# Performance work log

Hardware: AMD Instinct MI355X
Metric: run time of the kernel (lower is better)

The kernel has to match this reference:

```python
import jax, jax.numpy as jnp
import numpy as np

B, SEQ_LEN, IN_DIM = 16, 1024, 768
R = 0.1
PI = 3.1415926


def conv1d(x, w, b):
    # x: [B,C,L], w: [O,I,3], 'same' padding, stride 1
    y = jax.lax.conv_general_dilated(x, w, window_strides=(1,), padding=[(1, 1)],
                                     dimension_numbers=('NCH', 'OIH', 'NCH'))
    return y + b[None, :, None]


def layernorm_cl(x, g, b, eps=1e-5):
    # torch nn.LayerNorm((C, L)): normalize jointly over the last two dims of [B,C,L]
    m = x.mean(axis=(1, 2), keepdims=True)
    v = x.var(axis=(1, 2), keepdims=True)
    return (x - m) / jnp.sqrt(v + eps) * g[None] + b[None]


def setup_inputs() -> dict:
    key = jax.random.key(0)
    ks = jax.random.split(key, 8)
    D, D2, L = IN_DIM, IN_DIM * 2, SEQ_LEN
    sc1 = 1.0 / np.sqrt(D * 3)
    sc2 = 1.0 / np.sqrt(D2 * 3)
    return {
        'feats': jax.random.normal(ks[0], (B, L, D), dtype=jnp.float32),
        'conv1_w': jax.random.normal(ks[1], (D2, D, 3), dtype=jnp.float32) * sc1,
        'conv1_b': jnp.zeros((D2,), jnp.float32),
        'ln1_w': jnp.ones((D2, L), jnp.float32),
        'ln1_b': jnp.zeros((D2, L), jnp.float32),
        'conv2_w': jax.random.normal(ks[2], (D2, D2, 3), dtype=jnp.float32) * sc2,
        'conv2_b': jnp.zeros((D2,), jnp.float32),
        'ln2_w': jnp.ones((D2, L), jnp.float32),
        'ln2_b': jnp.zeros((D2, L), jnp.float32),
        'conv3_w': jax.random.normal(ks[3], (2, D2, 3), dtype=jnp.float32) * sc2,
        'conv3_b': jnp.zeros((2,), jnp.float32),
        'ln3_w': jnp.ones((2, L), jnp.float32),
        'ln3_b': jnp.zeros((2, L), jnp.float32),
    }


def reference(feats, conv1_w, conv1_b, ln1_w, ln1_b, conv2_w, conv2_b, ln2_w, ln2_b,
              conv3_w, conv3_b, ln3_w, ln3_b):
    # NOTE: original uses nn.LeakyReLU(True) -> negative_slope=1.0, i.e. identity.
    x = jnp.transpose(feats, (0, 2, 1))                 # [B,D,L]
    h = layernorm_cl(conv1d(x, conv1_w, conv1_b), ln1_w, ln1_b)
    h = layernorm_cl(conv1d(h, conv2_w, conv2_b), ln2_w, ln2_b)
    h = layernorm_cl(conv1d(h, conv3_w, conv3_b), ln3_w, ln3_b)  # [B,2,L]
    s = jax.nn.softmax(h[:, 0, :], axis=1)              # [B,L]
    w = jax.nn.softmax(h[:, 1, :], axis=1)              # [B,L]
    # Vectorized over all centers i: std[b,i] = R*L*s[b,i]
    std = R * SEQ_LEN * s                               # [B,L]
    pos = jnp.arange(SEQ_LEN, dtype=feats.dtype)
    diff2 = (pos[None, :] - pos[:, None]) ** 2          # [i_center, j]
    c = (2.0 * PI) ** -0.5
    gauss = c / std[:, :, None] * jnp.exp(-diff2[None] / (1e-05 + 2.0 * std[:, :, None] ** 2))
    gauss = gauss / jnp.max(gauss, axis=2, keepdims=True)
    att = gauss * w[:, None, :]                         # [B,L_center,L]
    out = jnp.einsum('bij,bjd->bid', att, feats)        # [B,L,D]
    return out
```

## Files before the change

kernel.cpp:

```cpp
#include <hip/hip_runtime.h>
#include <hip/hip_bf16.h>
#include <cstdint>

#define B_   16
#define L_   1024
#define D_   768
#define D2_  1536

typedef __attribute__((ext_vector_type(8))) short bf16x8;
typedef __attribute__((ext_vector_type(4))) float f32x4;

__device__ __forceinline__ float ldin(const void* p, size_t i, int bf) {
  if (bf) return __bfloat162float(((const __hip_bfloat16*)p)[i]);
  return ((const float*)p)[i];
}
__device__ __forceinline__ unsigned short f2bs(float f) {
  __hip_bfloat16 h = __float2bfloat16(f);
  return *(unsigned short*)&h;
}
__device__ __forceinline__ float bs2f(unsigned short u) {
  __hip_bfloat16 h; *(unsigned short*)&h = u;
  return __bfloat162float(h);
}

__device__ __forceinline__ void gload16(const unsigned short* g, unsigned short* l) {
  __builtin_amdgcn_global_load_lds(
      (const __attribute__((address_space(1))) unsigned int*)g,
      (__attribute__((address_space(3))) unsigned int*)l, 16, 0, 0);
}

__global__ void k_detect(const void* __restrict__ ln1w, int* __restrict__ flag) {
  if (threadIdx.x == 0) {
    unsigned u = *(const unsigned*)ln1w;
    *flag = (u == 0x3F800000u) ? 0 : 1;
  }
}

__global__ __launch_bounds__(256) void k_cvt_x(const void* __restrict__ in,
                                               unsigned short* __restrict__ out,
                                               const int* __restrict__ flag) {
  const int bf = *flag;
  const size_t total = (size_t)B_ * (L_ + 2) * D_;
  for (size_t i = (size_t)blockIdx.x * 256 + threadIdx.x; i < total; i += (size_t)gridDim.x * 256) {
    size_t b = i / ((L_ + 2) * D_);
    size_t rem = i - b * ((size_t)(L_ + 2) * D_);
    int pr = (int)(rem / D_);
    int ci = (int)(rem - (size_t)pr * D_);
    float v = 0.f;
    if (pr >= 1 && pr <= L_) v = ldin(in, (b * L_ + pr - 1) * D_ + ci, bf);
    out[i] = f2bs(v);
  }
}

template<int IC>
__global__ __launch_bounds__(256) void k_cvt_w(const void* __restrict__ w,
                                               unsigned short* __restrict__ wp,
                                               const int* __restrict__ flag) {
  const int bf = *flag;
  const int n = D2_ * 3 * IC;
  for (int e = blockIdx.x * 256 + threadIdx.x; e < n; e += gridDim.x * 256) {
    int o = e / (3 * IC); int rem = e - o * 3 * IC;
    int t = rem / IC;     int ci = rem - t * IC;
    wp[e] = f2bs(ldin(w, ((size_t)o * IC + ci) * 3 + t, bf));
  }
}

__global__ __launch_bounds__(256) void k_cvt_lnp(const void* __restrict__ src,
                                                 unsigned short* __restrict__ dst,
                                                 const int* __restrict__ flag) {
  const int bf = *flag;
  __shared__ float t[32][33];
  const int l0 = blockIdx.x * 32, c0 = blockIdx.y * 32;
  const int tx = threadIdx.x, ty = threadIdx.y;
#pragma unroll
  for (int k = 0; k < 4; ++k)
    t[ty + k * 8][tx] = ldin(src, (size_t)(c0 + ty + k * 8) * L_ + l0 + tx, bf);
  __syncthreads();
#pragma unroll
  for (int k = 0; k < 4; ++k)
    dst[(size_t)(l0 + ty + k * 8) * D2_ + c0 + tx] = f2bs(t[tx][ty + k * 8]);
}

__global__ __launch_bounds__(256) void k_zero_hpad(unsigned short* __restrict__ hbp, int G) {
  int i = blockIdx.x * 256 + threadIdx.x;
  int per = 2 * D2_;
  if (i >= G * per) return;
  int lb = i / per; int rem = i - lb * per;
  int w = rem / D2_; int c = rem - w * D2_;
  hbp[((size_t)lb * (L_ + 2) + (size_t)w * (L_ + 1)) * D2_ + c] = 0;
}

template<int IC>
__global__ __launch_bounds__(512, 2) void k_conv_mfma(const unsigned short* __restrict__ x,
                                                      const unsigned short* __restrict__ wp,
                                                      const void* __restrict__ bias,
                                                      unsigned short* __restrict__ hout,
                                                      float* __restrict__ part,
                                                      const int* __restrict__ flag, int b0) {
  __shared__ __attribute__((aligned(16))) unsigned short Xs0[258 * 32];
  __shared__ __attribute__((aligned(16))) unsigned short Xs1[258 * 32];
  __shared__ __attribute__((aligned(16))) unsigned short Ws0[3 * 128 * 32];
  __shared__ __attribute__((aligned(16))) unsigned short Ws1[3 * 128 * 32];
  __shared__ float rs[8], rss[8];
  const int l0 = blockIdx.x * 256, o0 = blockIdx.y * 128, lb = blockIdx.z;
  const int tid = threadIdx.x;
  const int lane = tid & 63, wid = tid >> 6;
  const int wm = wid >> 1, wn = wid & 1;
  const int lr = lane & 15, lg = lane >> 4;

  f32x4 acc[4][4];
#pragma unroll
  for (int m = 0; m < 4; ++m)
#pragma unroll
    for (int n = 0; n < 4; ++n)
      acc[m][n] = (f32x4){0.f, 0.f, 0.f, 0.f};

  const int sx = ((1 + (tid >> 2)) >> 1) & 3;
  const int sw = ((tid >> 2) >> 1) & 3;
  const unsigned short* xbase = x + ((size_t)lb * (L_ + 2) + l0 + 1 + (tid >> 2)) * IC
                                  + (size_t)((tid & 3) ^ sx) * 8;
  const unsigned short* wbase = wp + (size_t)(o0 + (tid >> 2)) * 3 * IC
                                   + (size_t)((tid & 3) ^ sw) * 8;
  const int hr = (tid >> 2) * 257, hcs = tid & 3;
  const unsigned short* hbase = x + ((size_t)lb * (L_ + 2) + l0 + hr) * IC + hcs * 8;

  auto STAGE = [&](unsigned short* Xd, unsigned short* Wd, int ci) {
#pragma unroll
    for (int k = 0; k < 2; ++k)
      gload16(xbase + ci + (size_t)k * 128 * IC, Xd + 32 + tid * 8 + k * 4096);
#pragma unroll
    for (int k = 0; k < 3; ++k)
      gload16(wbase + ci + (size_t)k * IC, Wd + tid * 8 + k * 4096);
  };
  auto COMPUTE = [&](const unsigned short* Xd, const unsigned short* Wd) {
    const int pb = (((lr >> 1) & 3) ^ lg) * 8;
#pragma unroll
    for (int t = 0; t < 3; ++t) {
      const int pa = ((((lr + t) >> 1) & 3) ^ lg) * 8;
      bf16x8 b[4];
#pragma unroll
      for (int n = 0; n < 4; ++n)
        b[n] = *(const bf16x8*)&Wd[(t * 128 + wn * 64 + n * 16 + lr) * 32 + pb];
      __builtin_amdgcn_s_setprio(1);
#pragma unroll
      for (int m = 0; m < 4; ++m) {
        bf16x8 a = *(const bf16x8*)&Xd[(wm * 64 + m * 16 + lr + t) * 32 + pa];
#pragma unroll
        for (int n = 0; n < 4; ++n)
          acc[m][n] = __builtin_amdgcn_mfma_f32_16x16x32_bf16(a, b[n], acc[m][n], 0, 0, 0);
      }
      __builtin_amdgcn_s_setprio(0);
    }
  };

  bf16x8 hreg = {0, 0, 0, 0, 0, 0, 0, 0};
  if (tid < 8) hreg = *(const bf16x8*)(hbase + 0);
  STAGE(Xs0, Ws0, 0);
  if (tid < 8) *(bf16x8*)(Xs0 + hr * 32 + hcs * 8) = hreg;
  asm volatile("s_waitcnt vmcnt(0) lgkmcnt(0)" ::: "memory");
  __builtin_amdgcn_s_barrier();

  for (int ci0 = 0; ci0 < IC; ci0 += 64) {
    {
      const int cin = ci0 + 32;
      if (tid < 8) hreg = *(const bf16x8*)(hbase + cin);
      STAGE(Xs1, Ws1, cin);
      COMPUTE(Xs0, Ws0);
      if (tid < 8) *(bf16x8*)(Xs1 + hr * 32 + hcs * 8) = hreg;
      asm volatile("s_waitcnt vmcnt(0) lgkmcnt(0)" ::: "memory");
      __builtin_amdgcn_s_barrier();
    }
    {
      const int cin = ci0 + 64;
      const bool more = cin < IC;
      if (more) {
        if (tid < 8) hreg = *(const bf16x8*)(hbase + cin);
        STAGE(Xs0, Ws0, cin);
      }
      COMPUTE(Xs1, Ws1);
      if (more) {
        if (tid < 8) *(bf16x8*)(Xs0 + hr * 32 + hcs * 8) = hreg;
        asm volatile("s_waitcnt vmcnt(0) lgkmcnt(0)" ::: "memory");
        __builtin_amdgcn_s_barrier();
      }
    }
  }

  const int bf = *flag;
  float s = 0.f, ss = 0.f;
  unsigned short* hb = hout + ((size_t)lb * (L_ + 2) + 1) * D2_;
#pragma unroll
  for (int n = 0; n < 4; ++n) {
    int oo = o0 + wn * 64 + n * 16 + lr;
    float bv = ldin(bias, oo, bf);
#pragma unroll
    for (int m = 0; m < 4; ++m) {
      int lbase = l0 + wm * 64 + m * 16 + lg * 4;
#pragma unroll
      for (int j = 0; j < 4; ++j) {
        float v = acc[m][n][j] + bv;
        hb[(size_t)(lbase + j) * D2_ + oo] = f2bs(v);
        s += v; ss += v * v;
      }
    }
  }
#pragma unroll
  for (int o = 32; o > 0; o >>= 1) { s += __shfl_down(s, o); ss += __shfl_down(ss, o); }
  if (lane == 0) { rs[wid] = s; rss[wid] = ss; }
  __syncthreads();
  if (tid == 0) {
    float S = 0.f, SS = 0.f;
#pragma unroll
    for (int w = 0; w < 8; ++w) { S += rs[w]; SS += rss[w]; }
    size_t pi = ((size_t)(b0 + lb) * 48 + blockIdx.y * 4 + blockIdx.x) * 2;
    part[pi]     = S;
    part[pi + 1] = SS;
  }
}

__global__ void k_stats_final(const float* __restrict__ part, float* __restrict__ stat,
                              int NP, float invN, int b0) {
  const int b = b0 + blockIdx.x;
  float s = 0.f, ss = 0.f;
  for (int p = threadIdx.x; p < NP; p += blockDim.x) {
    s  += part[(size_t)(b * NP + p) * 2];
    ss += part[(size_t)(b * NP + p) * 2 + 1];
  }
#pragma unroll
  for (int o = 32; o > 0; o >>= 1) { s += __shfl_down(s, o); ss += __shfl_down(ss, o); }
  __shared__ float rs[2], rss[2];
  int lane = threadIdx.x & 63, wv = threadIdx.x >> 6;
  if (lane == 0) { rs[wv] = s; rss[wv] = ss; }
  __syncthreads();
  if (threadIdx.x == 0) {
    float m = (rs[0] + rs[1]) * invN;
    float var = (rss[0] + rss[1]) * invN - m * m;
    stat[b * 2] = m;
    stat[b * 2 + 1] = rsqrtf(var + 1e-5f);
  }
}

__global__ __launch_bounds__(256) void k_ln_inplace(unsigned short* __restrict__ hbp,
                                                    const unsigned short* __restrict__ gp,
                                                    const unsigned short* __restrict__ bp,
                                                    const float* __restrict__ stat, int b0) {
  const int lb = blockIdx.y;
  const float m = stat[(b0 + lb) * 2], rstd = stat[(b0 + lb) * 2 + 1];
  const int per8 = D2_ * L_ / 8;
  unsigned short* h = hbp + ((size_t)lb * (L_ + 2) + 1) * D2_;
  for (int e = blockIdx.x * 256 + threadIdx.x; e < per8; e += gridDim.x * 256) {
    bf16x8 v = *(bf16x8*)(h + (size_t)e * 8);
    bf16x8 g = *(const bf16x8*)(gp + (size_t)e * 8);
    bf16x8 bb = *(const bf16x8*)(bp + (size_t)e * 8);
    bf16x8 o;
#pragma unroll
    for (int j = 0; j < 8; ++j)
      o[j] = (short)f2bs((bs2f((unsigned short)v[j]) - m) * rstd * bs2f((unsigned short)g[j])
                         + bs2f((unsigned short)bb[j]));
    *(bf16x8*)(h + (size_t)e * 8) = o;
  }
}

__global__ __launch_bounds__(256) void k_conv3b(const unsigned short* __restrict__ hbp,
                                                const void* __restrict__ w3,
                                                const void* __restrict__ b3,
                                                float* __restrict__ y3,
                                                const int* __restrict__ flag, int b0) {
  __shared__ unsigned short w3s[2 * 3 * D2_];
  const int bf = *flag;
  const int lb = blockIdx.y, gb = b0 + lb;
  const int tid = threadIdx.x, lane = tid & 63, wid = tid >> 6;
  for (int e = tid; e < 2 * 3 * D2_; e += 256) {
    int ch = e / (3 * D2_); int rem = e - ch * 3 * D2_;
    int t = rem / D2_;      int c = rem - t * D2_;
    w3s[e] = f2bs(ldin(w3, ((size_t)ch * D2_ + c) * 3 + t, bf));
  }
  __syncthreads();
  const int l = blockIdx.x * 4 + wid;
  float a0 = 0.f, a1 = 0.f;
#pragma unroll
  for (int t = 0; t < 3; ++t) {
    const unsigned short* hr = hbp + ((size_t)lb * (L_ + 2) + l + t) * D2_;
    const unsigned short* w0 = w3s + t * D2_;
    const unsigned short* w1 = w3s + (3 + t) * D2_;
#pragma unroll
    for (int i = 0; i < 3; ++i) {
      int c0 = (i * 64 + lane) * 8;
      bf16x8 hv  = *(const bf16x8*)(hr + c0);
      bf16x8 wv0 = *(const bf16x8*)(w0 + c0);
      bf16x8 wv1 = *(const bf16x8*)(w1 + c0);
#pragma unroll
      for (int j = 0; j < 8; ++j) {
        float h = bs2f((unsigned short)hv[j]);
        a0 += h * bs2f((unsigned short)wv0[j]);
        a1 += h * bs2f((unsigned short)wv1[j]);
      }
    }
  }
#pragma unroll
  for (int o = 32; o > 0; o >>= 1) { a0 += __shfl_down(a0, o); a1 += __shfl_down(a1, o); }
  if (lane == 0) {
    y3[((size_t)gb * 2) * L_ + l]     = a0 + ldin(b3, 0, bf);
    y3[((size_t)gb * 2 + 1) * L_ + l] = a1 + ldin(b3, 1, bf);
  }
}

__global__ void k_stats3(const float* __restrict__ y3, float* __restrict__ stat3, int b0) {
  const int b = b0 + blockIdx.x;
  const float* p = y3 + (size_t)b * 2 * L_;
  float s = 0.f, ss = 0.f;
  for (int i = threadIdx.x; i < 2 * L_; i += 256) { float v = p[i]; s += v; ss += v * v; }
#pragma unroll
  for (int o = 32; o > 0; o >>= 1) { s += __shfl_down(s, o); ss += __shfl_down(ss, o); }
  __shared__ float rs[4], rss[4];
  int lane = threadIdx.x & 63, wv = threadIdx.x >> 6;
  if (lane == 0) { rs[wv] = s; rss[wv] = ss; }
  __syncthreads();
  if (threadIdx.x == 0) {
    float invN = 1.f / (2 * L_);
    float m = (rs[0] + rs[1] + rs[2] + rs[3]) * invN;
    float var = (rss[0] + rss[1] + rss[2] + rss[3]) * invN - m * m;
    stat3[b * 2] = m;
    stat3[b * 2 + 1] = rsqrtf(var + 1e-5f);
  }
}

__global__ __launch_bounds__(256) void k_softmax(const float* __restrict__ y3,
                                                 const void* __restrict__ g,
                                                 const void* __restrict__ bt,
                                                 const float* __restrict__ stat3,
                                                 float* __restrict__ sw,
                                                 const int* __restrict__ flag, int b0) {
  const int bf = *flag;
  const int ch = blockIdx.x, gb = b0 + blockIdx.y, tid = threadIdx.x;
  const float m = stat3[gb * 2], rstd = stat3[gb * 2 + 1];
  const float* yp = y3 + ((size_t)gb * 2 + ch) * L_;
  float z[4];
  float mx = -1e30f;
#pragma unroll
  for (int k = 0; k < 4; ++k) {
    int l = tid + k * 256;
    z[k] = (yp[l] - m) * rstd * ldin(g, (size_t)ch * L_ + l, bf) + ldin(bt, (size_t)ch * L_ + l, bf);
    mx = fmaxf(mx, z[k]);
  }
#pragma unroll
  for (int o = 32; o > 0; o >>= 1) mx = fmaxf(mx, __shfl_xor(mx, o));
  __shared__ float red[4];
  int lane = tid & 63, wv = tid >> 6;
  if (lane == 0) red[wv] = mx;
  __syncthreads();
  mx = fmaxf(fmaxf(red[0], red[1]), fmaxf(red[2], red[3]));
  float e[4], sum = 0.f;
#pragma unroll
  for (int k = 0; k < 4; ++k) { e[k] = __expf(z[k] - mx); sum += e[k]; }
#pragma unroll
  for (int o = 32; o > 0; o >>= 1) sum += __shfl_xor(sum, o);
  __shared__ float red2[4];
  if (lane == 0) red2[wv] = sum;
  __syncthreads();
  sum = red2[0] + red2[1] + red2[2] + red2[3];
  float inv = 1.f / sum;
#pragma unroll
  for (int k = 0; k < 4; ++k) {
    int l = tid + k * 256;
    sw[((size_t)ch * B_ + gb) * L_ + l] = e[k] * inv;
  }
}

__global__ __launch_bounds__(256) void k_attn(const float* __restrict__ sw,
                                              const void* __restrict__ feats,
                                              void* __restrict__ out,
                                              const int* __restrict__ flag) {
  const int i = blockIdx.x, b = blockIdx.y, tid = threadIdx.x;
  const float s = sw[(size_t)b * L_ + i];
  const float* wv = sw + (size_t)B_ * L_ + (size_t)b * L_;
  const float stdv = 102.4f * s;
  const float denom = 1e-5f + 2.f * stdv * stdv;
  const float inv = 1.f / denom;
  int r = (int)ceilf(sqrtf(30.f * denom));
  int jlo = i - r; if (jlo < 0) jlo = 0;
  int jhi = i + r; if (jhi > L_ - 1) jhi = L_ - 1;
  float a0 = 0.f, a1 = 0.f, a2 = 0.f;
  const int bf = *flag;
  if (bf) {
    const __hip_bfloat16* fb = (const __hip_bfloat16*)feats + (size_t)b * L_ * D_ + tid;
    for (int j = jlo; j <= jhi; ++j) {
      float d = (float)(j - i);
      float gz = __expf(-d * d * inv) * wv[j];
      const __hip_bfloat16* f = fb + (size_t)j * D_;
      a0 += gz * __bfloat162float(f[0]);
      a1 += gz * __bfloat162float(f[256]);
      a2 += gz * __bfloat162float(f[512]);
    }
    __hip_bfloat16* op = (__hip_bfloat16*)out + ((size_t)b * L_ + i) * D_ + tid;
    op[0]   = __float2bfloat16(a0);
    op[256] = __float2bfloat16(a1);
    op[512] = __float2bfloat16(a2);
  } else {
    const float* fb = (const float*)feats + (size_t)b * L_ * D_ + tid;
    for (int j = jlo; j <= jhi; ++j) {
      float d = (float)(j - i);
      float gz = __expf(-d * d * inv) * wv[j];
      const float* f = fb + (size_t)j * D_;
      a0 += gz * f[0];
      a1 += gz * f[256];
      a2 += gz * f[512];
    }
    float* op = (float*)out + ((size_t)b * L_ + i) * D_ + tid;
    op[0] = a0; op[256] = a1; op[512] = a2;
  }
}

extern "C" void kernel_launch(void* const* d_in, const int* in_sizes, int n_in,
                              void* d_out, int out_size, void* d_ws, size_t ws_size,
                              hipStream_t stream) {
  (void)in_sizes; (void)n_in; (void)out_size;
  char* wsb = (char*)d_ws;
  size_t off = 0;
  auto alloc = [&](size_t bytes) -> char* {
    char* p = wsb + off;
    off += (bytes + 255) & ~(size_t)255;
    return p;
  };
  unsigned short* xbp  = (unsigned short*)alloc((size_t)B_ * (L_ + 2) * D_ * 2);
  unsigned short* wp1  = (unsigned short*)alloc((size_t)D2_ * 3 * D_ * 2);
  unsigned short* wp2  = (unsigned short*)alloc((size_t)D2_ * 3 * D2_ * 2);
  unsigned short* lp1w = (unsigned short*)alloc((size_t)D2_ * L_ * 2);
  unsigned short* lp1b = (unsigned short*)alloc((size_t)D2_ * L_ * 2);
  unsigned short* lp2w = (unsigned short*)alloc((size_t)D2_ * L_ * 2);
  unsigned short* lp2b = (unsigned short*)alloc((size_t)D2_ * L_ * 2);
  float* y3   = (float*)alloc((size_t)B_ * 2 * L_ * 4);
  float* swb  = (float*)alloc((size_t)2 * B_ * L_ * 4);
  float* part = (float*)alloc((size_t)B_ * 48 * 2 * 4);
  float* stat = (float*)alloc((size_t)B_ * 2 * 4);
  float* st3  = (float*)alloc((size_t)B_ * 2 * 4);
  int*   flag = (int*)alloc(16);
  const size_t fixed = off;

  int G = 1;
  const int cand[5] = {16, 8, 4, 2, 1};
  for (int k = 0; k < 5; ++k) {
    size_t need = fixed + (size_t)cand[k] * (size_t)(L_ + 2) * D2_ * 2 * 2 + 1024;
    if (need <= ws_size) { G = cand[k]; break; }
  }
  unsigned short* Hbp1 = (unsigned short*)alloc((size_t)G * (L_ + 2) * D2_ * 2);
  unsigned short* Hbp2 = (unsigned short*)alloc((size_t)G * (L_ + 2) * D2_ * 2);

  k_detect<<<1, 64, 0, stream>>>(d_in[3], flag);

  k_cvt_x<<<2048, 256, 0, stream>>>(d_in[0], xbp, flag);
  k_cvt_w<768><<<2048, 256, 0, stream>>>(d_in[1], wp1, flag);
  k_cvt_w<1536><<<2048, 256, 0, stream>>>(d_in[5], wp2, flag);
  dim3 tg(32, 48), tb(32, 8);
  k_cvt_lnp<<<tg, tb, 0, stream>>>(d_in[3], lp1w, flag);
  k_cvt_lnp<<<tg, tb, 0, stream>>>(d_in[4], lp1b, flag);
  k_cvt_lnp<<<tg, tb, 0, stream>>>(d_in[7], lp2w, flag);
  k_cvt_lnp<<<tg, tb, 0, stream>>>(d_in[8], lp2b, flag);
  k_zero_hpad<<<(G * 2 * D2_ + 255) / 256, 256, 0, stream>>>(Hbp1, G);
  k_zero_hpad<<<(G * 2 * D2_ + 255) / 256, 256, 0, stream>>>(Hbp2, G);

  const float invN = 1.f / (float)(D2_ * L_);
  for (int b0 = 0; b0 < B_; b0 += G) {
    k_conv_mfma<768><<<dim3(4, 12, G), 512, 0, stream>>>(
        xbp + (size_t)b0 * (L_ + 2) * D_, wp1, d_in[2], Hbp1, part, flag, b0);
    k_stats_final<<<G, 128, 0, stream>>>(part, stat, 48, invN, b0);
    k_ln_inplace<<<dim3(768, G), 256, 0, stream>>>(Hbp1, lp1w, lp1b, stat, b0);

    k_conv_mfma<1536><<<dim3(4, 12, G), 512, 0, stream>>>(
        Hbp1, wp2, d_in[6], Hbp2, part, flag, b0);
    k_stats_final<<<G, 128, 0, stream>>>(part, stat, 48, invN, b0);
    k_ln_inplace<<<dim3(768, G), 256, 0, stream>>>(Hbp2, lp2w, lp2b, stat, b0);

    k_conv3b<<<dim3(L_ / 4, G), 256, 0, stream>>>(Hbp2, d_in[9], d_in[10], y3, flag, b0);
    k_stats3<<<G, 256, 0, stream>>>(y3, st3, b0);
    k_softmax<<<dim3(2, G), 256, 0, stream>>>(y3, d_in[11], d_in[12], st3, swb, flag, b0);
  }

  k_attn<<<dim3(L_, B_), 256, 0, stream>>>(swb, d_in[0], d_out, flag);
}
```

Before: 490.1 us.

## Fold identity LayerNorm into following conv epilogue when affine params are trivial

A device-side check tests whether all LayerNorm gamma/beta tensors are exactly ones/zeros. When they are, the in-place LayerNorm passes and the LN-param conversions are skipped. The mean/rstd normalization is instead folded algebraically into the epilogue of the next convolution, using precomputed per-output tap sums of the weights with boundary corrections at l=0 and l=L-1. This removes two full read/write passes over the large intermediate activations per batch group. In exchange it adds a full scan of the LN parameters and a poorly coalesced weight-sum kernel. It also convolves unnormalized bf16 activations, which may shift numerical error.

```diff
diff --git a/kernel.cpp b/kernel.cpp
--- a/kernel.cpp
+++ b/kernel.cpp
@@ -32,7 +32,66 @@
 __global__ void k_detect(const void* __restrict__ ln1w, int* __restrict__ flag) {
   if (threadIdx.x == 0) {
     unsigned u = *(const unsigned*)ln1w;
-    *flag = (u == 0x3F800000u) ? 0 : 1;
+    flag[0] = (u == 0x3F800000u) ? 0 : 1;
+    flag[1] = 1;
+  }
+}
+
+__global__ __launch_bounds__(256) void k_check_lnp(const void* __restrict__ g1,
+                                                   const void* __restrict__ b1,
+                                                   const void* __restrict__ g2,
+                                                   const void* __restrict__ b2,
+                                                   const void* __restrict__ g3,
+                                                   const void* __restrict__ b3,
+                                                   const int* __restrict__ flag,
+                                                   int* __restrict__ flag2) {
+  const int bf = *flag;
+  const int n = D2_ * L_;
+  bool bad = false;
+  for (int i = blockIdx.x * 256 + threadIdx.x; i < n; i += gridDim.x * 256) {
+    if (ldin(g1, i, bf) != 1.f || ldin(b1, i, bf) != 0.f ||
+        ldin(g2, i, bf) != 1.f || ldin(b2, i, bf) != 0.f) { bad = true; break; }
+    if (i < 2 * L_ && (ldin(g3, i, bf) != 1.f || ldin(b3, i, bf) != 0.f)) { bad = true; break; }
+  }
+  if (bad) atomicAnd(flag2, 0);
+}
+
+template<int IC>
+__global__ __launch_bounds__(256) void k_wsum(const void* __restrict__ w,
+                                              float* __restrict__ wt,
+                                              const int* __restrict__ flag) {
+  const int bf = *flag;
+  int o = blockIdx.x * 256 + threadIdx.x;
+  if (o >= D2_) return;
+  float s0 = 0.f, s1 = 0.f, s2 = 0.f;
+  for (int ci = 0; ci < IC; ++ci) {
+    size_t base = ((size_t)o * IC + ci) * 3;
+    s0 += ldin(w, base + 0, bf);
+    s1 += ldin(w, base + 1, bf);
+    s2 += ldin(w, base + 2, bf);
+  }
+  wt[o] = s0; wt[D2_ + o] = s1; wt[2 * D2_ + o] = s2;
+}
+
+__global__ void k_wsum3(const void* __restrict__ w3, float* __restrict__ wt3,
+                        const int* __restrict__ flag) {
+  const int bf = *flag;
+  const int tid = threadIdx.x;
+  float acc[6] = {0.f, 0.f, 0.f, 0.f, 0.f, 0.f};
+  for (int c = tid; c < D2_; c += 256)
+#pragma unroll
+    for (int ch = 0; ch < 2; ++ch)
+#pragma unroll
+      for (int t = 0; t < 3; ++t)
+        acc[ch * 3 + t] += ldin(w3, ((size_t)ch * D2_ + c) * 3 + t, bf);
+  __shared__ float red[6][256];
+#pragma unroll
+  for (int k = 0; k < 6; ++k) red[k][tid] = acc[k];
+  __syncthreads();
+  if (tid < 6) {
+    float s = 0.f;
+    for (int i = 0; i < 256; ++i) s += red[tid][i];
+    wt3[tid] = s;
   }
 }
 
@@ -67,7 +126,9 @@
 
 __global__ __launch_bounds__(256) void k_cvt_lnp(const void* __restrict__ src,
                                                  unsigned short* __restrict__ dst,
-                                                 const int* __restrict__ flag) {
+                                                 const int* __restrict__ flag,
+                                                 const int* __restrict__ flag2) {
+  if (*flag2) return;
   const int bf = *flag;
   __shared__ float t[32][33];
   const int l0 = blockIdx.x * 32, c0 = blockIdx.y * 32;
@@ -90,13 +151,16 @@
   hbp[((size_t)lb * (L_ + 2) + (size_t)w * (L_ + 1)) * D2_ + c] = 0;
 }
 
-template<int IC>
+template<int IC, bool FOLD>
 __global__ __launch_bounds__(512, 2) void k_conv_mfma(const unsigned short* __restrict__ x,
                                                       const unsigned short* __restrict__ wp,
                                                       const void* __restrict__ bias,
                                                       unsigned short* __restrict__ hout,
                                                       float* __restrict__ part,
-                                                      const int* __restrict__ flag, int b0) {
+                                                      const float* __restrict__ statp,
+                                                      const float* __restrict__ wt,
+                                                      const int* __restrict__ flag,
+                                                      const int* __restrict__ flag2, int b0) {
   __shared__ __attribute__((aligned(16))) unsigned short Xs0[258 * 32];
   __shared__ __attribute__((aligned(16))) unsigned short Xs1[258 * 32];
   __shared__ __attribute__((aligned(16))) unsigned short Ws0[3 * 128 * 32];
@@ -187,19 +251,41 @@
   }
 
   const int bf = *flag;
+  const bool fold = FOLD && (*flag2 != 0);
+  float r1 = 1.f, m1r = 0.f;
+  if (fold) {
+    float m1 = statp[(b0 + lb) * 2];
+    r1 = statp[(b0 + lb) * 2 + 1];
+    m1r = -m1 * r1;
+  }
   float s = 0.f, ss = 0.f;
   unsigned short* hb = hout + ((size_t)lb * (L_ + 2) + 1) * D2_;
 #pragma unroll
   for (int n = 0; n < 4; ++n) {
     int oo = o0 + wn * 64 + n * 16 + lr;
     float bv = ldin(bias, oo, bf);
+    float w0 = 0.f, w2 = 0.f, csum = 0.f;
+    if (fold) {
+      w0 = m1r * wt[oo];
+      w2 = m1r * wt[2 * D2_ + oo];
+      csum = w0 + m1r * wt[D2_ + oo] + w2;
+    }
 #pragma unroll
     for (int m = 0; m < 4; ++m) {
       int lbase = l0 + wm * 64 + m * 16 + lg * 4;
 #pragma unroll
       for (int j = 0; j < 4; ++j) {
-        float v = acc[m][n][j] + bv;
-        hb[(size_t)(lbase + j) * D2_ + oo] = f2bs(v);
+        int l = lbase + j;
+        float v;
+        if (fold) {
+          float c = csum;
+          if (l == 0) c -= w0;
+          if (l == L_ - 1) c -= w2;
+          v = r1 * acc[m][n][j] + c + bv;
+        } else {
+          v = acc[m][n][j] + bv;
+        }
+        hb[(size_t)l * D2_ + oo] = f2bs(v);
         s += v; ss += v * v;
       }
     }
@@ -243,7 +329,9 @@
 __global__ __launch_bounds__(256) void k_ln_inplace(unsigned short* __restrict__ hbp,
                                                     const unsigned short* __restrict__ gp,
                                                     const unsigned short* __restrict__ bp,
-                                                    const float* __restrict__ stat, int b0) {
+                                                    const float* __restrict__ stat,
+                                                    const int* __restrict__ flag2, int b0) {
+  if (*flag2) return;
   const int lb = blockIdx.y;
   const float m = stat[(b0 + lb) * 2], rstd = stat[(b0 + lb) * 2 + 1];
   const int per8 = D2_ * L_ / 8;
@@ -265,7 +353,10 @@
                                                 const void* __restrict__ w3,
                                                 const void* __restrict__ b3,
                                                 float* __restrict__ y3,
-                                                const int* __restrict__ flag, int b0) {
+                                                const float* __restrict__ stat,
+                                                const float* __restrict__ wt3,
+                                                const int* __restrict__ flag,
+                                                const int* __restrict__ flag2, int b0) {
   __shared__ unsigned short w3s[2 * 3 * D2_];
   const int bf = *flag;
   const int lb = blockIdx.y, gb = b0 + lb;
@@ -300,8 +391,23 @@
 #pragma unroll
   for (int o = 32; o > 0; o >>= 1) { a0 += __shfl_down(a0, o); a1 += __shfl_down(a1, o); }
   if (lane == 0) {
-    y3[((size_t)gb * 2) * L_ + l]     = a0 + ldin(b3, 0, bf);
-    y3[((size_t)gb * 2 + 1) * L_ + l] = a1 + ldin(b3, 1, bf);
+    float bv0 = ldin(b3, 0, bf), bv1 = ldin(b3, 1, bf);
+    float v0, v1;
+    if (*flag2) {
+      float m2 = stat[gb * 2], r2 = stat[gb * 2 + 1];
+      float m2r = -m2 * r2;
+      float c0 = m2r * (wt3[0] + wt3[1] + wt3[2]);
+      float c1 = m2r * (wt3[3] + wt3[4] + wt3[5]);
+      if (l == 0)      { c0 -= m2r * wt3[0]; c1 -= m2r * wt3[3]; }
+      if (l == L_ - 1) { c0 -= m2r * wt3[2]; c1 -= m2r * wt3[5]; }
+      v0 = r2 * a0 + c0 + bv0;
+      v1 = r2 * a1 + c1 + bv1;
+    } else {
+      v0 = a0 + bv0;
+      v1 = a1 + bv1;
+    }
+    y3[((size_t)gb * 2) * L_ + l]     = v0;
+    y3[((size_t)gb * 2 + 1) * L_ + l] = v1;
   }
 }
 
@@ -434,7 +540,10 @@
   float* part = (float*)alloc((size_t)B_ * 48 * 2 * 4);
   float* stat = (float*)alloc((size_t)B_ * 2 * 4);
   float* st3  = (float*)alloc((size_t)B_ * 2 * 4);
+  float* wt2  = (float*)alloc((size_t)3 * D2_ * 4);
+  float* wt3  = (float*)alloc(6 * 4);
   int*   flag = (int*)alloc(16);
+  int*   flag2 = flag + 1;
   const size_t fixed = off;
 
   int G = 1;
@@ -447,31 +556,37 @@
   unsigned short* Hbp2 = (unsigned short*)alloc((size_t)G * (L_ + 2) * D2_ * 2);
 
   k_detect<<<1, 64, 0, stream>>>(d_in[3], flag);
+  k_check_lnp<<<1024, 256, 0, stream>>>(d_in[3], d_in[4], d_in[7], d_in[8],
+                                        d_in[11], d_in[12], flag, flag2);
 
   k_cvt_x<<<2048, 256, 0, stream>>>(d_in[0], xbp, flag);
   k_cvt_w<768><<<2048, 256, 0, stream>>>(d_in[1], wp1, flag);
   k_cvt_w<1536><<<2048, 256, 0, stream>>>(d_in[5], wp2, flag);
+  k_wsum<1536><<<6, 256, 0, stream>>>(d_in[5], wt2, flag);
+  k_wsum3<<<1, 256, 0, stream>>>(d_in[9], wt3, flag);
   dim3 tg(32, 48), tb(32, 8);
-  k_cvt_lnp<<<tg, tb, 0, stream>>>(d_in[3], lp1w, flag);
-  k_cvt_lnp<<<tg, tb, 0, stream>>>(d_in[4], lp1b, flag);
-  k_cvt_lnp<<<tg, tb, 0, stream>>>(d_in[7], lp2w, flag);
-  k_cvt_lnp<<<tg, tb, 0, stream>>>(d_in[8], lp2b, flag);
+  k_cvt_lnp<<<tg, tb, 0, stream>>>(d_in[3], lp1w, flag, flag2);
+  k_cvt_lnp<<<tg, tb, 0, stream>>>(d_in[4], lp1b, flag, flag2);
+  k_cvt_lnp<<<tg, tb, 0, stream>>>(d_in[7], lp2w, flag, flag2);
+  k_cvt_lnp<<<tg, tb, 0, stream>>>(d_in[8], lp2b, flag, flag2);
   k_zero_hpad<<<(G * 2 * D2_ + 255) / 256, 256, 0, stream>>>(Hbp1, G);
   k_zero_hpad<<<(G * 2 * D2_ + 255) / 256, 256, 0, stream>>>(Hbp2, G);
 
   const float invN = 1.f / (float)(D2_ * L_);
   for (int b0 = 0; b0 < B_; b0 += G) {
-    k_conv_mfma<768><<<dim3(4, 12, G), 512, 0, stream>>>(
-        xbp + (size_t)b0 * (L_ + 2) * D_, wp1, d_in[2], Hbp1, part, flag, b0);
+    k_conv_mfma<768, false><<<dim3(4, 12, G), 512, 0, stream>>>(
+        xbp + (size_t)b0 * (L_ + 2) * D_, wp1, d_in[2], Hbp1, part,
+        stat, wt2, flag, flag2, b0);
     k_stats_final<<<G, 128, 0, stream>>>(part, stat, 48, invN, b0);
-    k_ln_inplace<<<dim3(768, G), 256, 0, stream>>>(Hbp1, lp1w, lp1b, stat, b0);
-
-    k_conv_mfma<1536><<<dim3(4, 12, G), 512, 0, stream>>>(
-        Hbp1, wp2, d_in[6], Hbp2, part, flag, b0);
+    k_ln_inplace<<<dim3(768, G), 256, 0, stream>>>(Hbp1, lp1w, lp1b, stat, flag2, b0);
+
+    k_conv_mfma<1536, true><<<dim3(4, 12, G), 512, 0, stream>>>(
+        Hbp1, wp2, d_in[6], Hbp2, part, stat, wt2, flag, flag2, b0);
     k_stats_final<<<G, 128, 0, stream>>>(part, stat, 48, invN, b0);
-    k_ln_inplace<<<dim3(768, G), 256, 0, stream>>>(Hbp2, lp2w, lp2b, stat, b0);
-
-    k_conv3b<<<dim3(L_ / 4, G), 256, 0, stream>>>(Hbp2, d_in[9], d_in[10], y3, flag, b0);
+    k_ln_inplace<<<dim3(768, G), 256, 0, stream>>>(Hbp2, lp2w, lp2b, stat, flag2, b0);
+
+    k_conv3b<<<dim3(L_ / 4, G), 256, 0, stream>>>(Hbp2, d_in[9], d_in[10], y3,
+                                                  stat, wt3, flag, flag2, b0);
     k_stats3<<<G, 256, 0, stream>>>(y3, st3, b0);
     k_softmax<<<dim3(2, G), 256, 0, stream>>>(y3, d_in[11], d_in[12], st3, swb, flag, b0);
   }
```

After: 990.1 us. +102.0%, slower.
